# Kernel optimization log

Hardware: AMD Instinct MI355X
Metric: run time of the kernel (lower is better)

Reference implementation:

```python
import jax, jax.numpy as jnp
import numpy as np

D = 128
N = 262144

def setup_inputs() -> dict:
    key = jax.random.key(0)
    ks = jax.random.split(key, 10)
    inp = {
        'member_embeddings': 0.1 * jax.random.normal(ks[0], (N, D), dtype=jnp.float32),
        'item_embedding': 0.1 * jax.random.normal(ks[1], (D,), dtype=jnp.float32),
        # nn.Linear params (torch convention: y = x @ W.T + b)
        'W_c1': jax.random.normal(ks[2], (D, D), dtype=jnp.float32) / np.sqrt(D),
        'b_c1': jnp.zeros((D,), dtype=jnp.float32),
        'W_c2': jax.random.normal(ks[3], (D, D), dtype=jnp.float32) / np.sqrt(D),
        'b_c2': jnp.zeros((D,), dtype=jnp.float32),
        'w_pa': jax.random.normal(ks[4], (D,), dtype=jnp.float32) / np.sqrt(D),  # peer_attention weight (1,D) squeezed
        'b_pa': jnp.zeros((), dtype=jnp.float32),
        'w_vc': jax.random.normal(ks[5], (D,), dtype=jnp.float32) / np.sqrt(D),  # v_c weight (1,D) squeezed
        'b_vc': jnp.zeros((), dtype=jnp.float32),
    }
    return inp

def reference(member_embeddings, item_embedding, W_c1, b_c1, W_c2, b_c2, w_pa, b_pa, w_vc, b_vc):
    E = member_embeddings  # [N, D]
    # SP: self persistence scores  alpha_SP_i = u_i^T v
    sp = E @ item_embedding  # [N]
    # Peer scores are per-member scalars shared across all exclusion sets.
    s = E @ w_pa + b_pa                       # [N]
    m = jnp.max(s)
    e = jnp.exp(s - m)                        # [N]
    S = jnp.sum(e)                            # scalar
    eE = e[:, None] * E                       # [N, D]
    sum_eE = jnp.sum(eE, axis=0)              # [D]
    # softmax over peers excluding i (exact: softmax is shift-invariant)
    denom = S - e                             # [N]
    peer_agg = (sum_eE[None, :] - eE) / denom[:, None]  # [N, D]
    # PI: v_c^T ReLU(W_c1 u_i + W_c2 peer_agg_i + b)
    h = E @ W_c1.T + b_c1 + peer_agg @ W_c2.T + b_c2     # [N, D]
    pi = jax.nn.relu(h) @ w_vc + b_vc                    # [N]  (dropout = identity in eval)
    alpha = jnp.float32(1.0)
    beta = jnp.float32(1.0)
    attention_weights = jax.nn.softmax(alpha * sp + beta * pi, axis=0)  # [N]
    group_embedding = attention_weights @ E               # [D]
    return (group_embedding, attention_weights)
```

## Files before the change

### kernel.cpp

```cpp
#include <hip/hip_runtime.h>
#include <hip/hip_bf16.h>

#define DIM 128

typedef __attribute__((ext_vector_type(8))) short bf16x8;
typedef __attribute__((ext_vector_type(4))) float f32x4;

#define WS_B12    0
#define WS_C      128
#define WS_SUMEE  256
#define WS_S      384
#define WS_ZB     416
#define WS_GEB    512
#define WS_WBF    4608
#define WS_EEP    20992
#define WS_SEP    152064
#define WS_SP     153088
#define WS_E      415232
#define WS_WEXP   677376
#define WS_EBF    939520

__device__ __forceinline__ unsigned short f2bf(float f) {
    union { float f; unsigned u; } v; v.f = f;
    unsigned r = v.u + 0x7fffu + ((v.u >> 16) & 1u);
    return (unsigned short)(r >> 16);
}

__device__ __forceinline__ float bfbits(unsigned u) {
    union { unsigned u; float f; } v; v.u = u;
    return v.f;
}

__device__ __forceinline__ unsigned pkbf(float a, float b) {
    union { __hip_bfloat162 h; unsigned u; } cv;
    cv.h = __float22bfloat162_rn(make_float2(a, b));
    return cv.u;
}

__global__ __launch_bounds__(256) void k2_stats(const float* __restrict__ E,
                                                const float* __restrict__ v,
                                                const float* __restrict__ wpa,
                                                const float* __restrict__ bpa,
                                                const float* __restrict__ Wc1,
                                                const float* __restrict__ Wc2,
                                                const float* __restrict__ bc1,
                                                const float* __restrict__ bc2,
                                                float* __restrict__ ws) {
    __shared__ float red[16][128];
    __shared__ float redS[16];
    int t = threadIdx.x;

    int gid = blockIdx.x * 256 + t;
    unsigned short* wbf_w = (unsigned short*)(ws + WS_WBF);
    if (gid < 32768) {
        int n = gid >> 7, k = gid & 127;
        float val = (n < 128) ? Wc1[n * 128 + k] : Wc2[(n - 128) * 128 + k];
        wbf_w[gid] = f2bf(val);
    }
    if (gid < 4096) ws[WS_GEB + gid] = 0.f;
    if (gid < 128) ws[WS_B12 + gid] = bc1[gid] + bc2[gid];
    if (gid < 64) ws[WS_ZB + gid] = 0.f;

    int wave = t >> 6, lane = t & 63;
    int cl = lane & 15, rs = lane >> 4;
    int row0 = blockIdx.x * 256;
    const float4* E4 = (const float4*)E;
    unsigned short* ebf = (unsigned short*)(ws + WS_EBF);

    float4 va = ((const float4*)v)[cl];
    float4 vb = ((const float4*)v)[16 + cl];
    float4 pa = ((const float4*)wpa)[cl];
    float4 pb = ((const float4*)wpa)[16 + cl];
    float bias = bpa[0];

    float4 acc0 = {0.f, 0.f, 0.f, 0.f}, acc1 = {0.f, 0.f, 0.f, 0.f};
    float se = 0.f;
    float* sp_ws = ws + WS_SP;
    float* e_ws = ws + WS_E;

#pragma unroll 4
    for (int it = 0; it < 16; ++it) {
        int row = row0 + it * 16 + wave * 4 + rs;
        float4 x0 = E4[row * 32 + cl];
        float4 x1 = E4[row * 32 + 16 + cl];
        unsigned p0 = pkbf(x0.x, x0.y);
        unsigned p1 = pkbf(x0.z, x0.w);
        unsigned p2 = pkbf(x1.x, x1.y);
        unsigned p3 = pkbf(x1.z, x1.w);
        *(uint2*)(ebf + (size_t)row * 128 + cl * 4) = make_uint2(p0, p1);
        *(uint2*)(ebf + (size_t)row * 128 + 64 + cl * 4) = make_uint2(p2, p3);

        float dv = x0.x * va.x + x0.y * va.y + x0.z * va.z + x0.w * va.w
                 + x1.x * vb.x + x1.y * vb.y + x1.z * vb.z + x1.w * vb.w;
        float dp = x0.x * pa.x + x0.y * pa.y + x0.z * pa.z + x0.w * pa.w
                 + x1.x * pb.x + x1.y * pb.y + x1.z * pb.z + x1.w * pb.w;
        for (int off = 1; off < 16; off <<= 1) {
            dv += __shfl_xor(dv, off);
            dp += __shfl_xor(dp, off);
        }
        float e = __expf(dp + bias);
        if (cl == 0) {
            sp_ws[row] = dv;
            e_ws[row] = e;
            se += e;
        }
        acc0.x += e * x0.x; acc0.y += e * x0.y; acc0.z += e * x0.z; acc0.w += e * x0.w;
        acc1.x += e * x1.x; acc1.y += e * x1.y; acc1.z += e * x1.z; acc1.w += e * x1.w;
    }
    int rr = wave * 4 + rs;
    float* dst = red[rr];
    dst[cl * 4 + 0] = acc0.x; dst[cl * 4 + 1] = acc0.y;
    dst[cl * 4 + 2] = acc0.z; dst[cl * 4 + 3] = acc0.w;
    dst[64 + cl * 4 + 0] = acc1.x; dst[64 + cl * 4 + 1] = acc1.y;
    dst[64 + cl * 4 + 2] = acc1.z; dst[64 + cl * 4 + 3] = acc1.w;
    if (cl == 0) redS[rr] = se;
    __syncthreads();
    if (t < 128) {
        float s = 0.f;
#pragma unroll
        for (int r = 0; r < 16; ++r) s += red[r][t];
        ws[WS_EEP + t * 1024 + blockIdx.x] = s;
    }
    if (t == 0) {
        float s = 0.f;
#pragma unroll
        for (int r = 0; r < 16; ++r) s += redS[r];
        ws[WS_SEP + blockIdx.x] = s;
    }
}

__global__ __launch_bounds__(256) void k2b_reduce(float* __restrict__ ws) {
    __shared__ float r4[4];
    int t = threadIdx.x, blk = blockIdx.x;
    const float* src = (blk < 128) ? (ws + WS_EEP + blk * 1024) : (ws + WS_SEP);
    float s = src[t] + src[t + 256] + src[t + 512] + src[t + 768];
    for (int off = 1; off < 64; off <<= 1) s += __shfl_xor(s, off);
    if ((t & 63) == 0) r4[t >> 6] = s;
    __syncthreads();
    if (t == 0) {
        float tot = r4[0] + r4[1] + r4[2] + r4[3];
        if (blk < 128) ws[WS_SUMEE + blk] = tot;
        else ws[WS_S] = tot;
    }
}

__global__ __launch_bounds__(512, 4) void k4_main(const float* __restrict__ wvc,
                                                  const float* __restrict__ bvc_p,
                                                  const float* __restrict__ Wc2,
                                                  float* __restrict__ ws) {
    __shared__ unsigned short Elds[3][64 * 136];
    __shared__ __align__(16) float arena[1544];
    float* pim2  = arena;
    float* ed    = arena + 1024;
    float* c_lds = arena + 1408;
    float* zw    = arena + 1536;
    float* gep_a = arena;

    int t = threadIdx.x;
    int w = t >> 6, lane = t & 63, cl = lane & 15, q = lane >> 4;
    int blk = blockIdx.x;
    int row_base = blk * 256;
    const unsigned short* wbf = (const unsigned short*)(ws + WS_WBF);
    const unsigned short* EbBase = (const unsigned short*)(ws + WS_EBF);

    float bvc = bvc_p[0];
    float Sv = ws[WS_S];
    int r0 = w * 8 + q * 2;
    int sr = t >> 4, sc = t & 15;
    int sr1 = (t + 512) >> 4, sc1 = (t + 512) & 15;

    bf16x8 aw1[4], aw2[4];
#pragma unroll
    for (int kt = 0; kt < 4; ++kt) {
        aw1[kt] = *(const bf16x8*)(wbf + (w * 16 + cl) * 128 + kt * 32 + q * 8);
        aw2[kt] = *(const bf16x8*)(wbf + (128 + w * 16 + cl) * 128 + kt * 32 + q * 8);
    }

    float b12r[4], wvr[4];
#pragma unroll
    for (int reg = 0; reg < 4; ++reg) {
        int jr = w * 16 + q * 4 + reg;
        b12r[reg] = ws[WS_B12 + jr];
        wvr[reg] = wvc[jr];
    }

    if (t < 128) {
        const float4* row = (const float4*)(Wc2 + t * 128);
        const float4* se4 = (const float4*)(ws + WS_SUMEE);
        float4 s4 = {0.f, 0.f, 0.f, 0.f};
#pragma unroll
        for (int k = 0; k < 32; ++k) {
            float4 a = row[k], b = se4[k];
            s4.x += a.x * b.x; s4.y += a.y * b.y; s4.z += a.z * b.z; s4.w += a.w * b.w;
        }
        c_lds[t] = s4.x + s4.y + s4.z + s4.w;
    }

    {
        const unsigned short* Eb0 = EbBase + (size_t)row_base * 128;
        uint4 a0 = *(const uint4*)(Eb0 + t * 8);
        uint4 a1 = *(const uint4*)(Eb0 + (t + 512) * 8);
        *(uint4*)&Elds[0][sr * 136 + sc * 8] = a0;
        *(uint4*)&Elds[0][sr1 * 136 + sc1 * 8] = a1;
    }
    if (t < 64) {
        float ev = ws[WS_E + row_base + t];
        *(float2*)&ed[t * 2] = make_float2(ev, 1.0f / (Sv - ev));
    }
    uint4 sN0, sN1;
    float evN = 0.f;
    {
        const unsigned short* Eb1 = EbBase + (size_t)(row_base + 64) * 128;
        sN0 = *(const uint4*)(Eb1 + t * 8);
        sN1 = *(const uint4*)(Eb1 + (t + 512) * 8);
        if (t < 64) evN = ws[WS_E + row_base + 64 + t];
    }
    __syncthreads();

    float cjr[4];
#pragma unroll
    for (int reg = 0; reg < 4; ++reg) cjr[reg] = c_lds[w * 16 + q * 4 + reg];

    float z_lane = 0.f;
    float acc8[8] = {0.f, 0.f, 0.f, 0.f, 0.f, 0.f, 0.f, 0.f};

    for (int it = 0; it < 4; ++it) {
        int cur = it % 3;
        int pb = it & 1;
        int trow0 = row_base + it * 64;

        if (it < 3) {
            int wr = (it + 1) % 3;
            *(uint4*)&Elds[wr][sr * 136 + sc * 8] = sN0;
            *(uint4*)&Elds[wr][sr1 * 136 + sc1 * 8] = sN1;
            if (t < 64) *(float2*)&ed[(wr * 64 + t) * 2] = make_float2(evN, 1.0f / (Sv - evN));
        }
        if (it < 2) {
            const unsigned short* EbN = EbBase + (size_t)(trow0 + 128) * 128;
            sN0 = *(const uint4*)(EbN + t * 8);
            sN1 = *(const uint4*)(EbN + (t + 512) * 8);
            if (t < 64) evN = ws[WS_E + trow0 + 128 + t];
        }
        float sp0 = ws[WS_SP + trow0 + r0];
        float sp1 = ws[WS_SP + trow0 + r0 + 1];

        f32x4 acc[4][2];
#pragma unroll
        for (int rt = 0; rt < 4; ++rt) {
            acc[rt][0] = (f32x4){0.f, 0.f, 0.f, 0.f};
            acc[rt][1] = (f32x4){0.f, 0.f, 0.f, 0.f};
        }
#pragma unroll
        for (int rt = 0; rt < 4; ++rt) {
            bf16x8 b[4];
#pragma unroll
            for (int kt = 0; kt < 4; ++kt)
                b[kt] = *(const bf16x8*)&Elds[cur][(rt * 16 + cl) * 136 + kt * 32 + q * 8];
#pragma unroll
            for (int kt = 0; kt < 4; ++kt) {
                acc[rt][0] = __builtin_amdgcn_mfma_f32_16x16x32_bf16(aw1[kt], b[kt], acc[rt][0], 0, 0, 0);
                acc[rt][1] = __builtin_amdgcn_mfma_f32_16x16x32_bf16(aw2[kt], b[kt], acc[rt][1], 0, 0, 0);
            }
        }

#pragma unroll
        for (int rt = 0; rt < 4; ++rt) {
            float2 edv = *(const float2*)&ed[(cur * 64 + rt * 16 + cl) * 2];
            float p = 0.f;
#pragma unroll
            for (int reg = 0; reg < 4; ++reg) {
                float h = acc[rt][0][reg] + b12r[reg] + (cjr[reg] - edv.x * acc[rt][1][reg]) * edv.y;
                p = fmaf(wvr[reg], fmaxf(h, 0.f), p);
            }
            p += __shfl_xor(p, 16);
            p += __shfl_xor(p, 32);
            if (lane < 16) pim2[(pb * 64 + rt * 16 + lane) * 8 + w] = p;
        }
        __syncthreads();

        const float4* pr = (const float4*)&pim2[(pb * 64 + r0) * 8];
        float4 Pa = pr[0], Pb = pr[1], Pc = pr[2], Pd = pr[3];
        float pi0 = (Pa.x + Pa.y + Pa.z + Pa.w) + (Pb.x + Pb.y + Pb.z + Pb.w);
        float pi1 = (Pc.x + Pc.y + Pc.z + Pc.w) + (Pd.x + Pd.y + Pd.z + Pd.w);
        float we0 = __expf(sp0 + bvc + pi0);
        float we1 = __expf(sp1 + bvc + pi1);
        if (cl == 0) {
            ws[WS_WEXP + trow0 + r0] = we0;
            ws[WS_WEXP + trow0 + r0 + 1] = we1;
        }
        z_lane += we0 + we1;

#pragma unroll
        for (int rr = 0; rr < 2; ++rr) {
            int r = r0 + rr;
            float wer = rr ? we1 : we0;
            uint4 u = *(const uint4*)&Elds[cur][r * 136 + cl * 8];
            acc8[0] += wer * bfbits(u.x << 16);
            acc8[1] += wer * bfbits(u.x & 0xffff0000u);
            acc8[2] += wer * bfbits(u.y << 16);
            acc8[3] += wer * bfbits(u.y & 0xffff0000u);
            acc8[4] += wer * bfbits(u.z << 16);
            acc8[5] += wer * bfbits(u.z & 0xffff0000u);
            acc8[6] += wer * bfbits(u.w << 16);
            acc8[7] += wer * bfbits(u.w & 0xffff0000u);
        }
    }

    __syncthreads();

    z_lane += __shfl_xor(z_lane, 16);
    z_lane += __shfl_xor(z_lane, 32);
    if (lane == 0) zw[w] = z_lane;

#pragma unroll
    for (int jj = 0; jj < 8; ++jj) {
        acc8[jj] += __shfl_xor(acc8[jj], 16);
        acc8[jj] += __shfl_xor(acc8[jj], 32);
    }
    if (lane < 16) {
        *(float4*)&gep_a[w * 128 + cl * 8] = (float4){acc8[0], acc8[1], acc8[2], acc8[3]};
        *(float4*)&gep_a[w * 128 + cl * 8 + 4] = (float4){acc8[4], acc8[5], acc8[6], acc8[7]};
    }
    __syncthreads();

    if (t < 128) {
        float tot = 0.f;
#pragma unroll
        for (int wv = 0; wv < 8; ++wv) tot += gep_a[wv * 128 + t];
        atomicAdd(&ws[WS_GEB + (blk & 31) * 128 + t], tot);
    }
    if (t == 128) {
        float zs = zw[0] + zw[1] + zw[2] + zw[3] + zw[4] + zw[5] + zw[6] + zw[7];
        atomicAdd(&ws[WS_ZB + (blk & 63)], zs);
    }
}

__global__ __launch_bounds__(256) void k5_final(const float* __restrict__ ws,
                                                float* __restrict__ out) {
    int t = threadIdx.x, blk = blockIdx.x;
    float z = ws[WS_ZB + (t & 63)];
    for (int off = 1; off < 64; off <<= 1) z += __shfl_xor(z, off);
    float invZ = 1.0f / z;
    if (blk < 1024) {
        int i = blk * 256 + t;
        out[128 + i] = ws[WS_WEXP + i] * invZ;
    } else if (t < 128) {
        float s = 0.f;
#pragma unroll
        for (int b = 0; b < 32; ++b) s += ws[WS_GEB + b * 128 + t];
        out[t] = s * invZ;
    }
}

extern "C" void kernel_launch(void* const* d_in, const int* in_sizes, int n_in,
                              void* d_out, int out_size, void* d_ws, size_t ws_size,
                              hipStream_t stream) {
    const float* E   = (const float*)d_in[0];
    const float* v   = (const float*)d_in[1];
    const float* Wc1 = (const float*)d_in[2];
    const float* bc1 = (const float*)d_in[3];
    const float* Wc2 = (const float*)d_in[4];
    const float* bc2 = (const float*)d_in[5];
    const float* wpa = (const float*)d_in[6];
    const float* bpa = (const float*)d_in[7];
    const float* wvc = (const float*)d_in[8];
    const float* bvc = (const float*)d_in[9];
    float* ws  = (float*)d_ws;
    float* out = (float*)d_out;

    k2_stats<<<1024, 256, 0, stream>>>(E, v, wpa, bpa, Wc1, Wc2, bc1, bc2, ws);
    k2b_reduce<<<129, 256, 0, stream>>>(ws);
    k4_main<<<1024, 512, 0, stream>>>(wvc, bvc, Wc2, ws);
    k5_final<<<1025, 256, 0, stream>>>(ws, out);
}
```

Measured before the change: 264.5 us.

## Halve k4_main block to 4 waves, each computing 32 hidden columns

Reduces k4_main from 8 waves to 4 waves per block. Each wave now holds two 16-column weight tiles and computes 32 output features, so every E tile read from LDS feeds twice as many MFMAs. The cross-wave pi reduction, staging loads and final partial sums are resized to match. The cost is more registers per wave (twice the accumulators and weight fragments) and fewer waves in flight to hide memory latency.

Measured after the change: 259.9 us. About the same (-1.7%).

```diff
diff --git a/kernel.cpp b/kernel.cpp
--- a/kernel.cpp
+++ b/kernel.cpp
@@ -144,16 +144,16 @@
     }
 }
 
-__global__ __launch_bounds__(512, 4) void k4_main(const float* __restrict__ wvc,
+__global__ __launch_bounds__(256, 2) void k4_main(const float* __restrict__ wvc,
                                                   const float* __restrict__ bvc_p,
                                                   const float* __restrict__ Wc2,
                                                   float* __restrict__ ws) {
     __shared__ unsigned short Elds[3][64 * 136];
-    __shared__ __align__(16) float arena[1544];
+    __shared__ __align__(16) float arena[1028];
     float* pim2  = arena;
-    float* ed    = arena + 1024;
-    float* c_lds = arena + 1408;
-    float* zw    = arena + 1536;
+    float* ed    = arena + 512;
+    float* c_lds = arena + 896;
+    float* zw    = arena + 1024;
     float* gep_a = arena;
 
     int t = threadIdx.x;
@@ -165,24 +165,32 @@
 
     float bvc = bvc_p[0];
     float Sv = ws[WS_S];
-    int r0 = w * 8 + q * 2;
-    int sr = t >> 4, sc = t & 15;
-    int sr1 = (t + 512) >> 4, sc1 = (t + 512) & 15;
-
-    bf16x8 aw1[4], aw2[4];
-#pragma unroll
-    for (int kt = 0; kt < 4; ++kt) {
-        aw1[kt] = *(const bf16x8*)(wbf + (w * 16 + cl) * 128 + kt * 32 + q * 8);
-        aw2[kt] = *(const bf16x8*)(wbf + (128 + w * 16 + cl) * 128 + kt * 32 + q * 8);
-    }
-
-    float b12r[4], wvr[4];
-#pragma unroll
-    for (int reg = 0; reg < 4; ++reg) {
-        int jr = w * 16 + q * 4 + reg;
-        b12r[reg] = ws[WS_B12 + jr];
-        wvr[reg] = wvc[jr];
-    }
+    int r0 = w * 16 + q * 4;
+    int sr0 = t >> 4,           sc0 = t & 15;
+    int sr1 = (t + 256) >> 4,   sc1 = (t + 256) & 15;
+    int sr2 = (t + 512) >> 4,   sc2 = (t + 512) & 15;
+    int sr3 = (t + 768) >> 4,   sc3 = (t + 768) & 15;
+
+    bf16x8 aw[2][2][4];
+#pragma unroll
+    for (int jt = 0; jt < 2; ++jt) {
+#pragma unroll
+        for (int kt = 0; kt < 4; ++kt) {
+            int jrow = w * 32 + jt * 16 + cl;
+            aw[jt][0][kt] = *(const bf16x8*)(wbf + jrow * 128 + kt * 32 + q * 8);
+            aw[jt][1][kt] = *(const bf16x8*)(wbf + (128 + jrow) * 128 + kt * 32 + q * 8);
+        }
+    }
+
+    float b12r[2][4], wvr[2][4];
+#pragma unroll
+    for (int jt = 0; jt < 2; ++jt)
+#pragma unroll
+        for (int reg = 0; reg < 4; ++reg) {
+            int jr = w * 32 + jt * 16 + q * 4 + reg;
+            b12r[jt][reg] = ws[WS_B12 + jr];
+            wvr[jt][reg] = wvc[jr];
+        }
 
     if (t < 128) {
         const float4* row = (const float4*)(Wc2 + t * 128);
@@ -199,27 +207,36 @@
     {
         const unsigned short* Eb0 = EbBase + (size_t)row_base * 128;
         uint4 a0 = *(const uint4*)(Eb0 + t * 8);
-        uint4 a1 = *(const uint4*)(Eb0 + (t + 512) * 8);
-        *(uint4*)&Elds[0][sr * 136 + sc * 8] = a0;
+        uint4 a1 = *(const uint4*)(Eb0 + (t + 256) * 8);
+        uint4 a2 = *(const uint4*)(Eb0 + (t + 512) * 8);
+        uint4 a3 = *(const uint4*)(Eb0 + (t + 768) * 8);
+        *(uint4*)&Elds[0][sr0 * 136 + sc0 * 8] = a0;
         *(uint4*)&Elds[0][sr1 * 136 + sc1 * 8] = a1;
+        *(uint4*)&Elds[0][sr2 * 136 + sc2 * 8] = a2;
+        *(uint4*)&Elds[0][sr3 * 136 + sc3 * 8] = a3;
     }
     if (t < 64) {
         float ev = ws[WS_E + row_base + t];
         *(float2*)&ed[t * 2] = make_float2(ev, 1.0f / (Sv - ev));
     }
-    uint4 sN0, sN1;
+    uint4 sN0, sN1, sN2, sN3;
     float evN = 0.f;
     {
         const unsigned short* Eb1 = EbBase + (size_t)(row_base + 64) * 128;
         sN0 = *(const uint4*)(Eb1 + t * 8);
-        sN1 = *(const uint4*)(Eb1 + (t + 512) * 8);
+        sN1 = *(const uint4*)(Eb1 + (t + 256) * 8);
+        sN2 = *(const uint4*)(Eb1 + (t + 512) * 8);
+        sN3 = *(const uint4*)(Eb1 + (t + 768) * 8);
         if (t < 64) evN = ws[WS_E + row_base + 64 + t];
     }
     __syncthreads();
 
-    float cjr[4];
-#pragma unroll
-    for (int reg = 0; reg < 4; ++reg) cjr[reg] = c_lds[w * 16 + q * 4 + reg];
+    float cjr[2][4];
+#pragma unroll
+    for (int jt = 0; jt < 2; ++jt)
+#pragma unroll
+        for (int reg = 0; reg < 4; ++reg)
+            cjr[jt][reg] = c_lds[w * 32 + jt * 16 + q * 4 + reg];
 
     float z_lane = 0.f;
     float acc8[8] = {0.f, 0.f, 0.f, 0.f, 0.f, 0.f, 0.f, 0.f};
@@ -231,25 +248,30 @@
 
         if (it < 3) {
             int wr = (it + 1) % 3;
-            *(uint4*)&Elds[wr][sr * 136 + sc * 8] = sN0;
+            *(uint4*)&Elds[wr][sr0 * 136 + sc0 * 8] = sN0;
             *(uint4*)&Elds[wr][sr1 * 136 + sc1 * 8] = sN1;
+            *(uint4*)&Elds[wr][sr2 * 136 + sc2 * 8] = sN2;
+            *(uint4*)&Elds[wr][sr3 * 136 + sc3 * 8] = sN3;
             if (t < 64) *(float2*)&ed[(wr * 64 + t) * 2] = make_float2(evN, 1.0f / (Sv - evN));
         }
         if (it < 2) {
             const unsigned short* EbN = EbBase + (size_t)(trow0 + 128) * 128;
             sN0 = *(const uint4*)(EbN + t * 8);
-            sN1 = *(const uint4*)(EbN + (t + 512) * 8);
+            sN1 = *(const uint4*)(EbN + (t + 256) * 8);
+            sN2 = *(const uint4*)(EbN + (t + 512) * 8);
+            sN3 = *(const uint4*)(EbN + (t + 768) * 8);
             if (t < 64) evN = ws[WS_E + trow0 + 128 + t];
         }
-        float sp0 = ws[WS_SP + trow0 + r0];
-        float sp1 = ws[WS_SP + trow0 + r0 + 1];
-
-        f32x4 acc[4][2];
-#pragma unroll
-        for (int rt = 0; rt < 4; ++rt) {
-            acc[rt][0] = (f32x4){0.f, 0.f, 0.f, 0.f};
-            acc[rt][1] = (f32x4){0.f, 0.f, 0.f, 0.f};
-        }
+        float4 sp4 = *(const float4*)&ws[WS_SP + trow0 + r0];
+
+        f32x4 acc[4][2][2];
+#pragma unroll
+        for (int rt = 0; rt < 4; ++rt)
+#pragma unroll
+            for (int jt = 0; jt < 2; ++jt) {
+                acc[rt][jt][0] = (f32x4){0.f, 0.f, 0.f, 0.f};
+                acc[rt][jt][1] = (f32x4){0.f, 0.f, 0.f, 0.f};
+            }
 #pragma unroll
         for (int rt = 0; rt < 4; ++rt) {
             bf16x8 b[4];
@@ -258,8 +280,10 @@
                 b[kt] = *(const bf16x8*)&Elds[cur][(rt * 16 + cl) * 136 + kt * 32 + q * 8];
 #pragma unroll
             for (int kt = 0; kt < 4; ++kt) {
-                acc[rt][0] = __builtin_amdgcn_mfma_f32_16x16x32_bf16(aw1[kt], b[kt], acc[rt][0], 0, 0, 0);
-                acc[rt][1] = __builtin_amdgcn_mfma_f32_16x16x32_bf16(aw2[kt], b[kt], acc[rt][1], 0, 0, 0);
+                acc[rt][0][0] = __builtin_amdgcn_mfma_f32_16x16x32_bf16(aw[0][0][kt], b[kt], acc[rt][0][0], 0, 0, 0);
+                acc[rt][0][1] = __builtin_amdgcn_mfma_f32_16x16x32_bf16(aw[0][1][kt], b[kt], acc[rt][0][1], 0, 0, 0);
+                acc[rt][1][0] = __builtin_amdgcn_mfma_f32_16x16x32_bf16(aw[1][0][kt], b[kt], acc[rt][1][0], 0, 0, 0);
+                acc[rt][1][1] = __builtin_amdgcn_mfma_f32_16x16x32_bf16(aw[1][1][kt], b[kt], acc[rt][1][1], 0, 0, 0);
             }
         }
 
@@ -268,32 +292,35 @@
             float2 edv = *(const float2*)&ed[(cur * 64 + rt * 16 + cl) * 2];
             float p = 0.f;
 #pragma unroll
-            for (int reg = 0; reg < 4; ++reg) {
-                float h = acc[rt][0][reg] + b12r[reg] + (cjr[reg] - edv.x * acc[rt][1][reg]) * edv.y;
-                p = fmaf(wvr[reg], fmaxf(h, 0.f), p);
-            }
+            for (int jt = 0; jt < 2; ++jt)
+#pragma unroll
+                for (int reg = 0; reg < 4; ++reg) {
+                    float h = acc[rt][jt][0][reg] + b12r[jt][reg]
+                            + (cjr[jt][reg] - edv.x * acc[rt][jt][1][reg]) * edv.y;
+                    p = fmaf(wvr[jt][reg], fmaxf(h, 0.f), p);
+                }
             p += __shfl_xor(p, 16);
             p += __shfl_xor(p, 32);
-            if (lane < 16) pim2[(pb * 64 + rt * 16 + lane) * 8 + w] = p;
+            if (lane < 16) pim2[(pb * 64 + rt * 16 + lane) * 4 + w] = p;
         }
         __syncthreads();
 
-        const float4* pr = (const float4*)&pim2[(pb * 64 + r0) * 8];
-        float4 Pa = pr[0], Pb = pr[1], Pc = pr[2], Pd = pr[3];
-        float pi0 = (Pa.x + Pa.y + Pa.z + Pa.w) + (Pb.x + Pb.y + Pb.z + Pb.w);
-        float pi1 = (Pc.x + Pc.y + Pc.z + Pc.w) + (Pd.x + Pd.y + Pd.z + Pd.w);
-        float we0 = __expf(sp0 + bvc + pi0);
-        float we1 = __expf(sp1 + bvc + pi1);
-        if (cl == 0) {
-            ws[WS_WEXP + trow0 + r0] = we0;
-            ws[WS_WEXP + trow0 + r0 + 1] = we1;
-        }
-        z_lane += we0 + we1;
-
-#pragma unroll
-        for (int rr = 0; rr < 2; ++rr) {
+        float we[4];
+#pragma unroll
+        for (int rr = 0; rr < 4; ++rr) {
+            float4 P = *(const float4*)&pim2[(pb * 64 + r0 + rr) * 4];
+            float pi = (P.x + P.y) + (P.z + P.w);
+            float spv = (rr == 0) ? sp4.x : (rr == 1) ? sp4.y : (rr == 2) ? sp4.z : sp4.w;
+            we[rr] = __expf(spv + bvc + pi);
+            z_lane += we[rr];
+        }
+        if (cl == 0)
+            *(float4*)&ws[WS_WEXP + trow0 + r0] = (float4){we[0], we[1], we[2], we[3]};
+
+#pragma unroll
+        for (int rr = 0; rr < 4; ++rr) {
             int r = r0 + rr;
-            float wer = rr ? we1 : we0;
+            float wer = we[rr];
             uint4 u = *(const uint4*)&Elds[cur][r * 136 + cl * 8];
             acc8[0] += wer * bfbits(u.x << 16);
             acc8[1] += wer * bfbits(u.x & 0xffff0000u);
@@ -324,13 +351,11 @@
     __syncthreads();
 
     if (t < 128) {
-        float tot = 0.f;
-#pragma unroll
-        for (int wv = 0; wv < 8; ++wv) tot += gep_a[wv * 128 + t];
+        float tot = gep_a[t] + gep_a[128 + t] + gep_a[256 + t] + gep_a[384 + t];
         atomicAdd(&ws[WS_GEB + (blk & 31) * 128 + t], tot);
     }
     if (t == 128) {
-        float zs = zw[0] + zw[1] + zw[2] + zw[3] + zw[4] + zw[5] + zw[6] + zw[7];
+        float zs = zw[0] + zw[1] + zw[2] + zw[3];
         atomicAdd(&ws[WS_ZB + (blk & 63)], zs);
     }
 }
@@ -370,6 +395,6 @@
 
     k2_stats<<<1024, 256, 0, stream>>>(E, v, wpa, bpa, Wc1, Wc2, bc1, bc2, ws);
     k2b_reduce<<<129, 256, 0, stream>>>(ws);
-    k4_main<<<1024, 512, 0, stream>>>(wvc, bvc, Wc2, ws);
+    k4_main<<<1024, 256, 0, stream>>>(wvc, bvc, Wc2, ws);
     k5_final<<<1025, 256, 0, stream>>>(ws, out);
 }
```
